# Performance work log

Measured on AMD Instinct MI355X. Metric: run time of the kernel, lower is better.

Reference implementation:

```python
import jax, jax.numpy as jnp
import numpy as np

GX, GY, NH = 480, 360, 32
EPS = 1e-5


def _bn(x, g, b):
    # torch BatchNorm1d training-mode stats over the point dimension
    m = jnp.mean(x, axis=0)
    v = jnp.mean((x - m) ** 2, axis=0)
    return g * (x - m) / jnp.sqrt(v + EPS) + b


def setup_inputs():
    key = jax.random.key(0)
    ks = jax.random.split(key, 24)
    B, N, F = 2, 120000, 7
    s = 0.02
    inp = {
        "pt_fea": jax.random.normal(ks[0], (B, N, F), jnp.float32),
        "xy_ind": jax.random.randint(ks[1], (B, N, 2), 0, 360, dtype=jnp.int32),
        "bn0_g": jnp.ones((7,), jnp.float32), "bn0_b": jnp.zeros((7,), jnp.float32),
        "W1": jax.random.normal(ks[2], (7, 64), jnp.float32) * s,  "b1": jnp.zeros((64,), jnp.float32),
        "bn1_g": jnp.ones((64,), jnp.float32), "bn1_b": jnp.zeros((64,), jnp.float32),
        "W2": jax.random.normal(ks[3], (64, 128), jnp.float32) * s, "b2": jnp.zeros((128,), jnp.float32),
        "bn2_g": jnp.ones((128,), jnp.float32), "bn2_b": jnp.zeros((128,), jnp.float32),
        "W3": jax.random.normal(ks[4], (128, 256), jnp.float32) * s, "b3": jnp.zeros((256,), jnp.float32),
        "bn3_g": jnp.ones((256,), jnp.float32), "bn3_b": jnp.zeros((256,), jnp.float32),
        "W4": jax.random.normal(ks[5], (256, 512), jnp.float32) * s, "b4": jnp.zeros((512,), jnp.float32),
        "W5": jax.random.normal(ks[6], (512, NH), jnp.float32) * s, "b5": jnp.zeros((NH,), jnp.float32),
    }
    return inp


def _forward_sample(fea, xy, bn0_g, bn0_b, W1, b1, bn1_g, bn1_b, W2, b2,
                    bn2_g, bn2_b, W3, b3, bn3_g, bn3_b, W4, b4, W5, b5):
    # Simplified PointNet: BN -> (Linear, BN, ReLU) x3 -> Linear
    x = _bn(fea, bn0_g, bn0_b)
    x = jax.nn.relu(_bn(x @ W1 + b1, bn1_g, bn1_b))
    x = jax.nn.relu(_bn(x @ W2 + b2, bn2_g, bn2_b))
    x = jax.nn.relu(_bn(x @ W3 + b3, bn3_g, bn3_b))
    x = x @ W4 + b4                              # [N, 512]
    # per-voxel segment max over flattened BEV cell id
    ids = xy[:, 0] * GY + xy[:, 1]               # [N]
    nseg = GX * GY
    seg = jax.ops.segment_max(x, ids, num_segments=nseg)   # [nseg, 512]
    cnt = jax.ops.segment_sum(jnp.ones(ids.shape[0], x.dtype), ids, num_segments=nseg)
    occ = (cnt > 0)[:, None]
    seg = jnp.where(occ, seg, 0.0)               # empty voxels -> 0 (scatter semantics)
    nh = jax.nn.relu(seg @ W5 + b5)              # fea_compression
    nh = jnp.where(occ, nh, 0.0)
    return nh.reshape(GX, GY, NH).transpose(2, 0, 1)  # [NH, GX, GY]


def reference(pt_fea, xy_ind, bn0_g, bn0_b, W1, b1, bn1_g, bn1_b, W2, b2,
              bn2_g, bn2_b, W3, b3, bn3_g, bn3_b, W4, b4, W5, b5):
    f = lambda fea, xy: _forward_sample(fea, xy, bn0_g, bn0_b, W1, b1, bn1_g, bn1_b,
                                        W2, b2, bn2_g, bn2_b, W3, b3, bn3_g, bn3_b,
                                        W4, b4, W5, b5)
    return jax.vmap(f)(pt_fea, xy_ind)           # [B, NH, GX, GY]
```

## Files before the change

### kernel.cpp

```cpp
#include <hip/hip_runtime.h>
#include <cstdint>

#define GXD 480
#define GYD 360
#define NHD 32
#define NPTS 120000
#define MPAD 120064
#define SEGR 129600
#define NSEG (GXD*GYD)
#define EPSB 1e-5f

using short8 = __attribute__((ext_vector_type(8))) short;
using f32x4  = __attribute__((ext_vector_type(4))) float;

__device__ __forceinline__ float bf2f(unsigned short u) {
    return __uint_as_float(((unsigned int)u) << 16);
}
__device__ __forceinline__ unsigned short f2bf(float f) {
    unsigned int u = __float_as_uint(f);
    u += 0x7fffu + ((u >> 16) & 1u);
    return (unsigned short)(u >> 16);
}
__device__ __forceinline__ unsigned int bnrelu_pack(unsigned int wv, float sc0, float sh0,
                                                    float sc1, float sh1)
{
    float lo = fmaxf(fmaf(bf2f((unsigned short)(wv & 0xffffu)), sc0, sh0), 0.f);
    float hi = fmaxf(fmaf(bf2f((unsigned short)(wv >> 16)), sc1, sh1), 0.f);
    return (unsigned int)f2bf(lo) | ((unsigned int)f2bf(hi) << 16);
}
__device__ __forceinline__ short8 bn_frag(short8 a, float4 s0, float4 s1,
                                          float4 h0, float4 h1)
{
    union { short8 v; uint4 u; } in, out;
    in.v = a;
    out.u.x = bnrelu_pack(in.u.x, s0.x, h0.x, s0.y, h0.y);
    out.u.y = bnrelu_pack(in.u.y, s0.z, h0.z, s0.w, h0.w);
    out.u.z = bnrelu_pack(in.u.z, s1.x, h1.x, s1.y, h1.y);
    out.u.w = bnrelu_pack(in.u.w, s1.z, h1.z, s1.w, h1.w);
    return out.v;
}

__device__ __forceinline__ void async16(const unsigned short* g, unsigned short* l)
{
    __builtin_amdgcn_global_load_lds(
        (const __attribute__((address_space(1))) unsigned int*)g,
        (__attribute__((address_space(3))) unsigned int*)l, 16, 0, 0);
}

__global__ __launch_bounds__(256) void bn0_stats_kernel(
    const float* __restrict__ fea, float* __restrict__ s0, float* __restrict__ q0)
{
    float s[7] = {0,0,0,0,0,0,0}, q[7] = {0,0,0,0,0,0,0};
    for (int p = blockIdx.x * 256 + threadIdx.x; p < NPTS; p += gridDim.x * 256) {
        const float* r = fea + (size_t)p * 7;
#pragma unroll
        for (int f = 0; f < 7; ++f) { float v = r[f]; s[f] += v; q[f] += v * v; }
    }
    __shared__ float red[256];
    int t = threadIdx.x;
#pragma unroll
    for (int f = 0; f < 7; ++f) {
        red[t] = s[f]; __syncthreads();
        for (int o = 128; o > 0; o >>= 1) {
            if (t < o) red[t] += red[t + o];
            __syncthreads();
        }
        if (t == 0) atomicAdd(&s0[f], red[0]);
        __syncthreads();
        red[t] = q[f]; __syncthreads();
        for (int o = 128; o > 0; o >>= 1) {
            if (t < o) red[t] += red[t + o];
            __syncthreads();
        }
        if (t == 0) atomicAdd(&q0[f], red[0]);
        __syncthreads();
    }
}

__global__ void prep0_kernel(const float* __restrict__ s0, const float* __restrict__ q0,
                             const float* __restrict__ g0, const float* __restrict__ b0,
                             const float* __restrict__ W1, const float* __restrict__ b1,
                             float* __restrict__ W1p, float* __restrict__ b1p)
{
    __shared__ float sc[7], sh[7];
    int t = threadIdx.x;
    if (t < 7) {
        float m = s0[t] / (float)NPTS;
        float v = q0[t] / (float)NPTS - m * m;
        float inv = 1.0f / sqrtf(fmaxf(v, 0.f) + EPSB);
        sc[t] = g0[t] * inv;
        sh[t] = b0[t] - m * g0[t] * inv;
    }
    __syncthreads();
    if (t < 64) {
        float acc = b1[t];
#pragma unroll
        for (int f = 0; f < 7; ++f) {
            W1p[f * 64 + t] = W1[f * 64 + t] * sc[f];
            acc += sh[f] * W1[f * 64 + t];
        }
        b1p[t] = acc;
    }
}

__global__ void prep_bn_kernel(const float* __restrict__ sum, const float* __restrict__ sq,
                               const float* __restrict__ g, const float* __restrict__ b,
                               float* __restrict__ sc, float* __restrict__ sh, int C)
{
    int c = blockIdx.x * blockDim.x + threadIdx.x;
    if (c < C) {
        float m = sum[c] / (float)NPTS;
        float v = sq[c] / (float)NPTS - m * m;
        float inv = 1.0f / sqrtf(fmaxf(v, 0.f) + EPSB);
        sc[c] = g[c] * inv;
        sh[c] = b[c] - m * g[c] * inv;
    }
}

__global__ __launch_bounds__(256) void wtrans_kernel(const float* __restrict__ W,
                                                     unsigned short* __restrict__ Wt,
                                                     int K, int N)
{
    int i = blockIdx.x * 256 + threadIdx.x;
    if (i < K * N) {
        int k = i / N, n = i % N;
        Wt[(size_t)n * K + k] = f2bf(W[i]);
    }
}

__global__ __launch_bounds__(256) void layer1_kernel(
    const float* __restrict__ fea, const float* __restrict__ W1p, const float* __restrict__ b1p,
    unsigned short* __restrict__ y1, float* __restrict__ sum1, float* __restrict__ sq1)
{
    __shared__ float Wl[448], bl[64];
    __shared__ float feaL[256 * 7];
    __shared__ float colsum[64], colsq[64];
    int t = threadIdx.x;
    int p0 = blockIdx.x * 256;
    for (int i = t; i < 448; i += 256) Wl[i] = W1p[i];
    if (t < 64) { bl[t] = b1p[t]; colsum[t] = 0.f; colsq[t] = 0.f; }
    int nval7 = (NPTS - p0) * 7;
    for (int i = t; i < 256 * 7; i += 256)
        feaL[i] = (i < nval7) ? fea[(size_t)p0 * 7 + i] : 0.f;
    __syncthreads();
    int cg = t & 7, pt = t >> 3;
    float s[8] = {}, q[8] = {};
#pragma unroll
    for (int it = 0; it < 8; ++it) {
        int row = it * 32 + pt;
        bool valid = (p0 + row) < NPTS;
        float f[7];
#pragma unroll
        for (int ff = 0; ff < 7; ++ff) f[ff] = feaL[row * 7 + ff];
        float vj[8];
#pragma unroll
        for (int j = 0; j < 8; ++j) {
            int c = cg * 8 + j;
            float v = bl[c];
#pragma unroll
            for (int ff = 0; ff < 7; ++ff) v = fmaf(f[ff], Wl[ff * 64 + c], v);
            vj[j] = v;
            if (valid) { s[j] += v; q[j] += v * v; }
        }
        uint4 ow;
        ow.x = (unsigned int)f2bf(vj[0]) | ((unsigned int)f2bf(vj[1]) << 16);
        ow.y = (unsigned int)f2bf(vj[2]) | ((unsigned int)f2bf(vj[3]) << 16);
        ow.z = (unsigned int)f2bf(vj[4]) | ((unsigned int)f2bf(vj[5]) << 16);
        ow.w = (unsigned int)f2bf(vj[6]) | ((unsigned int)f2bf(vj[7]) << 16);
        *(uint4*)(y1 + (size_t)(p0 + row) * 64 + cg * 8) = ow;
    }
#pragma unroll
    for (int off = 8; off < 64; off <<= 1) {
#pragma unroll
        for (int j = 0; j < 8; ++j) {
            s[j] += __shfl_xor(s[j], off);
            q[j] += __shfl_xor(q[j], off);
        }
    }
    if ((t & 63) < 8) {
#pragma unroll
        for (int j = 0; j < 8; ++j) {
            atomicAdd(&colsum[cg * 8 + j], s[j]);
            atomicAdd(&colsq[cg * 8 + j], q[j]);
        }
    }
    __syncthreads();
    if (t < 64) {
        atomicAdd(&sum1[t], colsum[t]);
        atomicAdd(&sq1[t], colsq[t]);
    }
}

template<int K, int NC, bool STATS>
__global__ __launch_bounds__(256) void gemm_quad(
    const unsigned short* __restrict__ A, const unsigned short* __restrict__ Wt,
    const float* __restrict__ scale, const float* __restrict__ shift,
    const float* __restrict__ bias, unsigned short* __restrict__ Y,
    float* __restrict__ osum, float* __restrict__ osq)
{
    __shared__ __align__(16) unsigned short lds[4 * 8192];
    __shared__ __align__(16) float scs[K], shs[K];
    __shared__ float colsum[128], colsq[128];
    int t = threadIdx.x;
    int w = t >> 6, ln = t & 63, quad = ln >> 4, lr = ln & 15;
    int wr = w >> 1, wc = w & 1;
    int mb = blockIdx.y * 128 + wr * 64;
    int cb = blockIdx.x * 128 + wc * 64;
    unsigned short* A0 = lds + w * 8192;
    unsigned short* B0 = A0 + 2048;
    unsigned short* A1 = A0 + 4096;
    unsigned short* B1 = A0 + 6144;

    for (int i = t; i < K; i += 256) { scs[i] = scale[i]; shs[i] = shift[i]; }
    if (STATS && t < 128) { colsum[t] = 0.f; colsq[t] = 0.f; }
    __syncthreads();

    const int grow = ln >> 2;
    const int swz = (((ln & 3) ^ ((ln >> 4) & 3)) << 3);
    const int rswz = ((quad ^ (lr >> 2)) << 3);

    f32x4 acc[4][4];
#pragma unroll
    for (int i = 0; i < 4; ++i)
#pragma unroll
        for (int j = 0; j < 4; ++j) acc[i][j] = (f32x4){0.f, 0.f, 0.f, 0.f};

#pragma unroll
    for (int i = 0; i < 4; ++i) {
        async16(A  + (size_t)(mb + i * 16 + grow) * K + swz, A0 + i * 512 + ln * 8);
        async16(Wt + (size_t)(cb + i * 16 + grow) * K + swz, B0 + i * 512 + ln * 8);
    }
#pragma unroll
    for (int i = 0; i < 4; ++i) {
        async16(A  + (size_t)(mb + i * 16 + grow) * K + 32 + swz, A1 + i * 512 + ln * 8);
        async16(Wt + (size_t)(cb + i * 16 + grow) * K + 32 + swz, B1 + i * 512 + ln * 8);
    }

#pragma unroll
    for (int r = 0; r < K / 32; ++r) {
        const int kt = r * 32;
        unsigned short* Acur = (r & 1) ? A1 : A0;
        unsigned short* Bcur = (r & 1) ? B1 : B0;
        int k0 = kt + quad * 8;
        float4 s0 = *(const float4*)&scs[k0];
        float4 s1 = *(const float4*)&scs[k0 + 4];
        float4 h0 = *(const float4*)&shs[k0];
        float4 h1 = *(const float4*)&shs[k0 + 4];
        if (r + 1 < K / 32)
            asm volatile("s_waitcnt vmcnt(8)" ::: "memory");
        else
            asm volatile("s_waitcnt vmcnt(0)" ::: "memory");
        short8 af[4], bfr[4];
#pragma unroll
        for (int mi = 0; mi < 4; ++mi)
            af[mi] = *(const short8*)&Acur[mi * 512 + lr * 32 + rswz];
#pragma unroll
        for (int ni = 0; ni < 4; ++ni)
            bfr[ni] = *(const short8*)&Bcur[ni * 512 + lr * 32 + rswz];
        asm volatile("s_waitcnt lgkmcnt(0)" ::: "memory");
        if (r + 2 < K / 32) {
            const int kn = kt + 64;
#pragma unroll
            for (int i = 0; i < 4; ++i) {
                async16(A  + (size_t)(mb + i * 16 + grow) * K + kn + swz,
                        Acur + i * 512 + ln * 8);
                async16(Wt + (size_t)(cb + i * 16 + grow) * K + kn + swz,
                        Bcur + i * 512 + ln * 8);
            }
        }
#pragma unroll
        for (int mi = 0; mi < 4; ++mi)
            af[mi] = bn_frag(af[mi], s0, s1, h0, h1);
#pragma unroll
        for (int mi = 0; mi < 4; ++mi)
#pragma unroll
            for (int ni = 0; ni < 4; ++ni)
                acc[mi][ni] = __builtin_amdgcn_mfma_f32_16x16x32_bf16(
                    af[mi], bfr[ni], acc[mi][ni], 0, 0, 0);
    }

    unsigned short* Cw = A0;
#pragma unroll
    for (int ni = 0; ni < 4; ++ni) {
        int col = ni * 16 + lr;
        float bv = bias[cb + col];
        float s = 0.f, q = 0.f;
#pragma unroll
        for (int mi = 0; mi < 4; ++mi) {
            int rb = mi * 16 + quad * 4;
#pragma unroll
            for (int r = 0; r < 4; ++r) {
                float v = acc[mi][ni][r] + bv;
                Cw[(rb + r) * 64 + col] = f2bf(v);
                if (STATS && (mb + rb + r) < NPTS) { s += v; q += v * v; }
            }
        }
        if (STATS) {
            atomicAdd(&colsum[wc * 64 + col], s);
            atomicAdd(&colsq[wc * 64 + col], q);
        }
    }
#pragma unroll
    for (int i = 0; i < 8; ++i) {
        int idx = i * 64 + ln;
        int row = idx >> 3, colq = (idx & 7) * 8;
        *(uint4*)(Y + (size_t)(mb + row) * NC + cb + colq) = *(const uint4*)&Cw[row * 64 + colq];
    }
    if (STATS) {
        __syncthreads();
        if (t < 128) {
            atomicAdd(&osum[blockIdx.x * 128 + t], colsum[t]);
            atomicAdd(&osq[blockIdx.x * 128 + t], colsq[t]);
        }
    }
}

__global__ __launch_bounds__(256) void hist_kernel(const int* __restrict__ xy,
                                                   int* __restrict__ cnt)
{
    int p = blockIdx.x * 256 + threadIdx.x;
    if (p < NPTS) {
        int id = xy[(size_t)p * 2] * GYD + xy[(size_t)p * 2 + 1];
        atomicAdd(&cnt[id], 1);
    }
}

__global__ __launch_bounds__(256) void scanA_kernel(const int* __restrict__ cnt,
                                                    int* __restrict__ csum)
{
    __shared__ int red[256];
    int t = threadIdx.x, base = blockIdx.x * 2048;
    int s = 0;
    for (int i = t; i < 2048; i += 256) {
        int idx = base + i;
        if (idx < SEGR) s += cnt[idx];
    }
    red[t] = s; __syncthreads();
    for (int o = 128; o > 0; o >>= 1) { if (t < o) red[t] += red[t + o]; __syncthreads(); }
    if (t == 0) csum[blockIdx.x] = red[0];
}

__global__ void scanB_kernel(int* __restrict__ csum, int* __restrict__ offs)
{
    if (threadIdx.x == 0) {
        int run = 0;
        for (int i = 0; i < 64; ++i) { int v = csum[i]; csum[i] = run; run += v; }
        offs[SEGR] = run;
    }
}

__global__ __launch_bounds__(256) void scanC_kernel(const int* __restrict__ cnt,
                                                    const int* __restrict__ csum,
                                                    int* __restrict__ offs,
                                                    int* __restrict__ cursor)
{
    __shared__ int red[256];
    int t = threadIdx.x, base = blockIdx.x * 2048;
    int v[8]; int s = 0;
#pragma unroll
    for (int i = 0; i < 8; ++i) {
        int idx = base + t * 8 + i;
        v[i] = (idx < SEGR) ? cnt[idx] : 0;
        s += v[i];
    }
    red[t] = s; __syncthreads();
    for (int o = 1; o < 256; o <<= 1) {
        int x = (t >= o) ? red[t - o] : 0;
        __syncthreads();
        red[t] += x;
        __syncthreads();
    }
    int run = red[t] - s + csum[blockIdx.x];
#pragma unroll
    for (int i = 0; i < 8; ++i) {
        int idx = base + t * 8 + i;
        if (idx < SEGR) { offs[idx] = run; cursor[idx] = run; }
        run += v[i];
    }
}

__global__ __launch_bounds__(256) void scatter_idx_kernel(const int* __restrict__ xy,
                                                          int* __restrict__ cursor,
                                                          int* __restrict__ order)
{
    int p = blockIdx.x * 256 + threadIdx.x;
    if (p < NPTS) {
        int id = xy[(size_t)p * 2] * GYD + xy[(size_t)p * 2 + 1];
        int pos = atomicAdd(&cursor[id], 1);
        order[pos] = p;
    }
}

__global__ __launch_bounds__(256) void segmax_l5_kernel(
    const unsigned short* __restrict__ y4g, const unsigned short* __restrict__ Wt5,
    const int* __restrict__ offs, const int* __restrict__ order,
    int g, float* __restrict__ E)
{
    __shared__ __align__(16) unsigned short seg[64 * 136];
    __shared__ __align__(16) unsigned short w5s[32 * 136];
    __shared__ int offs_s[65];
    int t = threadIdx.x;
    int c0 = blockIdx.x * 64;
    if (t < 65) offs_s[t] = offs[c0 + t];
    {
        int n = t >> 3, ko = (t & 7) * 16;
        *(uint4*)&w5s[n * 136 + ko]     = *(const uint4*)(Wt5 + (size_t)n * 512 + g * 128 + ko);
        *(uint4*)&w5s[n * 136 + ko + 8] = *(const uint4*)(Wt5 + (size_t)n * 512 + g * 128 + ko + 8);
    }
    __syncthreads();
    int cell = t >> 2, q = t & 3;
    float mx[32];
#pragma unroll
    for (int i = 0; i < 32; ++i) mx[i] = -3.0e38f;
    int jb = offs_s[cell], je = offs_s[cell + 1];
    for (int j = jb; j < je; ++j) {
        int p = order[j];
        const uint4* rp = (const uint4*)(y4g + (size_t)p * 128 + q * 32);
#pragma unroll
        for (int u = 0; u < 4; ++u) {
            uint4 vv = rp[u];
            unsigned int wv[4] = {vv.x, vv.y, vv.z, vv.w};
#pragma unroll
            for (int k2 = 0; k2 < 4; ++k2) {
                int idx = u * 8 + k2 * 2;
                mx[idx]     = fmaxf(mx[idx],     bf2f((unsigned short)(wv[k2] & 0xffffu)));
                mx[idx + 1] = fmaxf(mx[idx + 1], bf2f((unsigned short)(wv[k2] >> 16)));
            }
        }
    }
    bool empty = (jb == je);
#pragma unroll
    for (int i = 0; i < 16; ++i) {
        float lo = empty ? 0.f : mx[2 * i], hi = empty ? 0.f : mx[2 * i + 1];
        unsigned int pk = (unsigned int)f2bf(lo) | ((unsigned int)f2bf(hi) << 16);
        *(unsigned int*)&seg[cell * 136 + q * 32 + 2 * i] = pk;
    }
    __syncthreads();
    int lane = t & 63, w = t >> 6, quad = lane >> 4, lr = lane & 15;
    f32x4 acc[2];
    acc[0] = (f32x4){0.f, 0.f, 0.f, 0.f};
    acc[1] = (f32x4){0.f, 0.f, 0.f, 0.f};
#pragma unroll
    for (int kt = 0; kt < 4; ++kt) {
        short8 af = *(const short8*)&seg[(w * 16 + lr) * 136 + kt * 32 + quad * 8];
#pragma unroll
        for (int ni = 0; ni < 2; ++ni) {
            short8 bfr = *(const short8*)&w5s[(ni * 16 + lr) * 136 + kt * 32 + quad * 8];
            acc[ni] = __builtin_amdgcn_mfma_f32_16x16x32_bf16(af, bfr, acc[ni], 0, 0, 0);
        }
    }
#pragma unroll
    for (int ni = 0; ni < 2; ++ni) {
        int h = ni * 16 + lr;
#pragma unroll
        for (int r = 0; r < 4; ++r) {
            int cr = w * 16 + quad * 4 + r;
            float* ep = E + (size_t)(c0 + cr) * 32 + h;
            float v = acc[ni][r];
            if (g > 0) v += *ep;
            *ep = v;
        }
    }
}

__global__ __launch_bounds__(256) void out_kernel(
    const float* __restrict__ E, const int* __restrict__ cnt,
    const float* __restrict__ b5, float* __restrict__ out)
{
    int t = threadIdx.x;
    int c0 = blockIdx.x * 64;
    int lane = t & 63, hq = t >> 6;
    int cell = c0 + lane;
    if (c0 >= SEGR) {
#pragma unroll
        for (int j = 0; j < 8; ++j)
            out[(size_t)(hq * 8 + j) * NSEG + cell] = 0.f;
        return;
    }
    bool oc = cnt[cell] > 0;
    float4 e0 = *(const float4*)(E + (size_t)cell * 32 + hq * 8);
    float4 e1 = *(const float4*)(E + (size_t)cell * 32 + hq * 8 + 4);
    float r[8] = {e0.x, e0.y, e0.z, e0.w, e1.x, e1.y, e1.z, e1.w};
#pragma unroll
    for (int j = 0; j < 8; ++j) {
        float v = oc ? fmaxf(r[j] + b5[hq * 8 + j], 0.f) : 0.f;
        out[(size_t)(hq * 8 + j) * NSEG + cell] = v;
    }
}

extern "C" void kernel_launch(void* const* d_in, const int* in_sizes, int n_in,
                              void* d_out, int out_size, void* d_ws, size_t ws_size,
                              hipStream_t stream)
{
    const float* pt_fea = (const float*)d_in[0];
    const int*   xy_ind = (const int*)d_in[1];
    const float* bn0_g  = (const float*)d_in[2];
    const float* bn0_b  = (const float*)d_in[3];
    const float* W1     = (const float*)d_in[4];
    const float* b1     = (const float*)d_in[5];
    const float* bn1_g  = (const float*)d_in[6];
    const float* bn1_b  = (const float*)d_in[7];
    const float* W2     = (const float*)d_in[8];
    const float* b2     = (const float*)d_in[9];
    const float* bn2_g  = (const float*)d_in[10];
    const float* bn2_b  = (const float*)d_in[11];
    const float* W3     = (const float*)d_in[12];
    const float* b3     = (const float*)d_in[13];
    const float* bn3_g  = (const float*)d_in[14];
    const float* bn3_b  = (const float*)d_in[15];
    const float* W4     = (const float*)d_in[16];
    const float* b4     = (const float*)d_in[17];
    const float* W5     = (const float*)d_in[18];
    const float* b5     = (const float*)d_in[19];
    float* out = (float*)d_out;

    const size_t oY2   = 61472768;
    const size_t oE    = oY2 + (size_t)MPAD * 128 * 2;
    const size_t oCnt  = oE + (size_t)SEGR * 32 * 4;
    const size_t oOffs = oCnt + 518400;
    const size_t oCur  = oOffs + 518528;
    const size_t oOrd  = oCur + 518400;
    const size_t oCsum = oOrd + 480000;
    const size_t oSt   = oCsum + 512;
    const size_t oWt2  = oSt + 16384;
    const size_t oWt3  = oWt2 + 16384;
    const size_t oWt4  = oWt3 + 65536;
    const size_t oWt5  = oWt4 + 262144;

    unsigned short* y1   = (unsigned short*)d_ws;
    unsigned short* y3   = (unsigned short*)d_ws;
    unsigned short* y2   = (unsigned short*)((char*)d_ws + oY2);
    unsigned short* y4g  = (unsigned short*)((char*)d_ws + oY2);
    float*          E    = (float*)((char*)d_ws + oE);
    int*            cnt  = (int*)((char*)d_ws + oCnt);
    int*            offs = (int*)((char*)d_ws + oOffs);
    int*            cur  = (int*)((char*)d_ws + oCur);
    int*            ord  = (int*)((char*)d_ws + oOrd);
    int*            csum = (int*)((char*)d_ws + oCsum);
    float*          st   = (float*)((char*)d_ws + oSt);
    unsigned short* Wt2  = (unsigned short*)((char*)d_ws + oWt2);
    unsigned short* Wt3  = (unsigned short*)((char*)d_ws + oWt3);
    unsigned short* Wt4  = (unsigned short*)((char*)d_ws + oWt4);
    unsigned short* Wt5  = (unsigned short*)((char*)d_ws + oWt5);

    float* s0 = st + 0;     float* q0 = st + 8;
    float* W1p = st + 16;   float* b1p = st + 464;
    float* sum1 = st + 528; float* sq1 = st + 592; float* sc1 = st + 656; float* sh1 = st + 720;
    float* sum2 = st + 784; float* sq2 = st + 912; float* sc2 = st + 1040; float* sh2 = st + 1168;
    float* sum3 = st + 1296; float* sq3 = st + 1552; float* sc3 = st + 1808; float* sh3 = st + 2064;

    const int MB128 = MPAD / 128;

    wtrans_kernel<<<(64 * 128 + 255) / 256, 256, 0, stream>>>(W2, Wt2, 64, 128);
    wtrans_kernel<<<(128 * 256 + 255) / 256, 256, 0, stream>>>(W3, Wt3, 128, 256);
    wtrans_kernel<<<(256 * 512 + 255) / 256, 256, 0, stream>>>(W4, Wt4, 256, 512);
    wtrans_kernel<<<(512 * 32 + 255) / 256, 256, 0, stream>>>(W5, Wt5, 512, 32);

    for (int b = 0; b < 2; ++b) {
        const float* fea_b = pt_fea + (size_t)b * NPTS * 7;
        const int*   xy_b  = xy_ind + (size_t)b * NPTS * 2;
        float*       out_b = out + (size_t)b * NHD * NSEG;

        (void)hipMemsetAsync(st, 0, 2320 * sizeof(float), stream);
        (void)hipMemsetAsync(cnt, 0, (size_t)SEGR * 4, stream);

        bn0_stats_kernel<<<128, 256, 0, stream>>>(fea_b, s0, q0);
        prep0_kernel<<<1, 64, 0, stream>>>(s0, q0, bn0_g, bn0_b, W1, b1, W1p, b1p);
        layer1_kernel<<<MPAD / 256, 256, 0, stream>>>(fea_b, W1p, b1p, y1, sum1, sq1);
        prep_bn_kernel<<<1, 64, 0, stream>>>(sum1, sq1, bn1_g, bn1_b, sc1, sh1, 64);
        gemm_quad<64, 128, true><<<dim3(1, MB128), 256, 0, stream>>>(
            y1, Wt2, sc1, sh1, b2, y2, sum2, sq2);
        prep_bn_kernel<<<1, 128, 0, stream>>>(sum2, sq2, bn2_g, bn2_b, sc2, sh2, 128);
        gemm_quad<128, 256, true><<<dim3(2, MB128), 256, 0, stream>>>(
            y2, Wt3, sc2, sh2, b3, y3, sum3, sq3);
        prep_bn_kernel<<<1, 256, 0, stream>>>(sum3, sq3, bn3_g, bn3_b, sc3, sh3, 256);

        hist_kernel<<<(NPTS + 255) / 256, 256, 0, stream>>>(xy_b, cnt);
        scanA_kernel<<<64, 256, 0, stream>>>(cnt, csum);
        scanB_kernel<<<1, 64, 0, stream>>>(csum, offs);
        scanC_kernel<<<64, 256, 0, stream>>>(cnt, csum, offs, cur);
        scatter_idx_kernel<<<(NPTS + 255) / 256, 256, 0, stream>>>(xy_b, cur, ord);

        for (int g = 0; g < 4; ++g) {
            gemm_quad<256, 128, false><<<dim3(1, MB128), 256, 0, stream>>>(
                y3, Wt4 + (size_t)g * 128 * 256, sc3, sh3, b4 + g * 128, y4g,
                nullptr, nullptr);
            segmax_l5_kernel<<<SEGR / 64, 256, 0, stream>>>(y4g, Wt5, offs, ord, g, E);
        }
        out_kernel<<<NSEG / 64, 256, 0, stream>>>(E, cnt, b5, out_b);
    }
}
```

Measured before the change: 838.1 us.

## Move BN+ReLU out of GEMM prologue into standalone elementwise passes

Removes the per-fragment BN-scale/shift and ReLU from the GEMM inner loop and instead applies BN+ReLU in place on y1, y2 and y3 with a new vectorized elementwise kernel. This also drops the LDS XOR swizzle in the GEMM and uses a packed bf16 convert instruction. The aim is to shorten the MFMA loop, especially since y3 was re-normalized four times across the W4 column groups. In exchange it adds extra full read/write passes over the activations and may bring back LDS bank conflicts now that the swizzle is gone.

```diff
diff --git a/kernel.cpp b/kernel.cpp
--- a/kernel.cpp
+++ b/kernel.cpp
@@ -24,20 +24,13 @@
 __device__ __forceinline__ unsigned int bnrelu_pack(unsigned int wv, float sc0, float sh0,
                                                     float sc1, float sh1)
 {
-    float lo = fmaxf(fmaf(bf2f((unsigned short)(wv & 0xffffu)), sc0, sh0), 0.f);
-    float hi = fmaxf(fmaf(bf2f((unsigned short)(wv >> 16)), sc1, sh1), 0.f);
-    return (unsigned int)f2bf(lo) | ((unsigned int)f2bf(hi) << 16);
-}
-__device__ __forceinline__ short8 bn_frag(short8 a, float4 s0, float4 s1,
-                                          float4 h0, float4 h1)
-{
-    union { short8 v; uint4 u; } in, out;
-    in.v = a;
-    out.u.x = bnrelu_pack(in.u.x, s0.x, h0.x, s0.y, h0.y);
-    out.u.y = bnrelu_pack(in.u.y, s0.z, h0.z, s0.w, h0.w);
-    out.u.z = bnrelu_pack(in.u.z, s1.x, h1.x, s1.y, h1.y);
-    out.u.w = bnrelu_pack(in.u.w, s1.z, h1.z, s1.w, h1.w);
-    return out.v;
+    float lo = __uint_as_float(wv << 16);
+    float hi = __uint_as_float(wv & 0xffff0000u);
+    lo = fmaxf(fmaf(lo, sc0, sh0), 0.f);
+    hi = fmaxf(fmaf(hi, sc1, sh1), 0.f);
+    unsigned int r;
+    asm("v_cvt_pk_bf16_f32 %0, %1, %2" : "=v"(r) : "v"(lo), "v"(hi));
+    return r;
 }
 
 __device__ __forceinline__ void async16(const unsigned short* g, unsigned short* l)
@@ -114,6 +107,32 @@
         float inv = 1.0f / sqrtf(fmaxf(v, 0.f) + EPSB);
         sc[c] = g[c] * inv;
         sh[c] = b[c] - m * g[c] * inv;
+    }
+}
+
+template<int C>
+__global__ __launch_bounds__(256) void bnrelu_kernel(
+    unsigned short* __restrict__ Y,
+    const float* __restrict__ sc, const float* __restrict__ sh)
+{
+    __shared__ float scs[C], shs[C];
+    int t = threadIdx.x;
+    for (int i = t; i < C; i += 256) { scs[i] = sc[i]; shs[i] = sh[i]; }
+    __syncthreads();
+    const size_t total8 = (size_t)MPAD * C / 8;
+    for (size_t i = (size_t)blockIdx.x * 256 + t; i < total8; i += (size_t)gridDim.x * 256) {
+        int c0 = (int)((i * 8) & (size_t)(C - 1));
+        uint4 v = *(const uint4*)(Y + i * 8);
+        float4 s0 = *(const float4*)&scs[c0];
+        float4 s1 = *(const float4*)&scs[c0 + 4];
+        float4 h0 = *(const float4*)&shs[c0];
+        float4 h1 = *(const float4*)&shs[c0 + 4];
+        uint4 o;
+        o.x = bnrelu_pack(v.x, s0.x, h0.x, s0.y, h0.y);
+        o.y = bnrelu_pack(v.y, s0.z, h0.z, s0.w, h0.w);
+        o.z = bnrelu_pack(v.z, s1.x, h1.x, s1.y, h1.y);
+        o.w = bnrelu_pack(v.w, s1.z, h1.z, s1.w, h1.w);
+        *(uint4*)(Y + i * 8) = o;
     }
 }
 
@@ -194,12 +213,10 @@
 template<int K, int NC, bool STATS>
 __global__ __launch_bounds__(256) void gemm_quad(
     const unsigned short* __restrict__ A, const unsigned short* __restrict__ Wt,
-    const float* __restrict__ scale, const float* __restrict__ shift,
     const float* __restrict__ bias, unsigned short* __restrict__ Y,
     float* __restrict__ osum, float* __restrict__ osq)
 {
     __shared__ __align__(16) unsigned short lds[4 * 8192];
-    __shared__ __align__(16) float scs[K], shs[K];
     __shared__ float colsum[128], colsq[128];
     int t = threadIdx.x;
     int w = t >> 6, ln = t & 63, quad = ln >> 4, lr = ln & 15;
@@ -211,13 +228,11 @@
     unsigned short* A1 = A0 + 4096;
     unsigned short* B1 = A0 + 6144;
 
-    for (int i = t; i < K; i += 256) { scs[i] = scale[i]; shs[i] = shift[i]; }
     if (STATS && t < 128) { colsum[t] = 0.f; colsq[t] = 0.f; }
     __syncthreads();
 
     const int grow = ln >> 2;
-    const int swz = (((ln & 3) ^ ((ln >> 4) & 3)) << 3);
-    const int rswz = ((quad ^ (lr >> 2)) << 3);
+    const int koff = (ln & 3) * 8;
 
     f32x4 acc[4][4];
 #pragma unroll
@@ -227,13 +242,13 @@
 
 #pragma unroll
     for (int i = 0; i < 4; ++i) {
-        async16(A  + (size_t)(mb + i * 16 + grow) * K + swz, A0 + i * 512 + ln * 8);
-        async16(Wt + (size_t)(cb + i * 16 + grow) * K + swz, B0 + i * 512 + ln * 8);
+        async16(A  + (size_t)(mb + i * 16 + grow) * K + koff, A0 + i * 512 + ln * 8);
+        async16(Wt + (size_t)(cb + i * 16 + grow) * K + koff, B0 + i * 512 + ln * 8);
     }
 #pragma unroll
     for (int i = 0; i < 4; ++i) {
-        async16(A  + (size_t)(mb + i * 16 + grow) * K + 32 + swz, A1 + i * 512 + ln * 8);
-        async16(Wt + (size_t)(cb + i * 16 + grow) * K + 32 + swz, B1 + i * 512 + ln * 8);
+        async16(A  + (size_t)(mb + i * 16 + grow) * K + 32 + koff, A1 + i * 512 + ln * 8);
+        async16(Wt + (size_t)(cb + i * 16 + grow) * K + 32 + koff, B1 + i * 512 + ln * 8);
     }
 
 #pragma unroll
@@ -241,11 +256,6 @@
         const int kt = r * 32;
         unsigned short* Acur = (r & 1) ? A1 : A0;
         unsigned short* Bcur = (r & 1) ? B1 : B0;
-        int k0 = kt + quad * 8;
-        float4 s0 = *(const float4*)&scs[k0];
-        float4 s1 = *(const float4*)&scs[k0 + 4];
-        float4 h0 = *(const float4*)&shs[k0];
-        float4 h1 = *(const float4*)&shs[k0 + 4];
         if (r + 1 < K / 32)
             asm volatile("s_waitcnt vmcnt(8)" ::: "memory");
         else
@@ -253,24 +263,21 @@
         short8 af[4], bfr[4];
 #pragma unroll
         for (int mi = 0; mi < 4; ++mi)
-            af[mi] = *(const short8*)&Acur[mi * 512 + lr * 32 + rswz];
+            af[mi] = *(const short8*)&Acur[mi * 512 + lr * 32 + quad * 8];
 #pragma unroll
         for (int ni = 0; ni < 4; ++ni)
-            bfr[ni] = *(const short8*)&Bcur[ni * 512 + lr * 32 + rswz];
+            bfr[ni] = *(const short8*)&Bcur[ni * 512 + lr * 32 + quad * 8];
         asm volatile("s_waitcnt lgkmcnt(0)" ::: "memory");
         if (r + 2 < K / 32) {
             const int kn = kt + 64;
 #pragma unroll
             for (int i = 0; i < 4; ++i) {
-                async16(A  + (size_t)(mb + i * 16 + grow) * K + kn + swz,
+                async16(A  + (size_t)(mb + i * 16 + grow) * K + kn + koff,
                         Acur + i * 512 + ln * 8);
-                async16(Wt + (size_t)(cb + i * 16 + grow) * K + kn + swz,
+                async16(Wt + (size_t)(cb + i * 16 + grow) * K + kn + koff,
                         Bcur + i * 512 + ln * 8);
             }
         }
-#pragma unroll
-        for (int mi = 0; mi < 4; ++mi)
-            af[mi] = bn_frag(af[mi], s0, s1, h0, h1);
 #pragma unroll
         for (int mi = 0; mi < 4; ++mi)
 #pragma unroll
@@ -568,12 +575,15 @@
         prep0_kernel<<<1, 64, 0, stream>>>(s0, q0, bn0_g, bn0_b, W1, b1, W1p, b1p);
         layer1_kernel<<<MPAD / 256, 256, 0, stream>>>(fea_b, W1p, b1p, y1, sum1, sq1);
         prep_bn_kernel<<<1, 64, 0, stream>>>(sum1, sq1, bn1_g, bn1_b, sc1, sh1, 64);
+        bnrelu_kernel<64><<<1024, 256, 0, stream>>>(y1, sc1, sh1);
         gemm_quad<64, 128, true><<<dim3(1, MB128), 256, 0, stream>>>(
-            y1, Wt2, sc1, sh1, b2, y2, sum2, sq2);
+            y1, Wt2, b2, y2, sum2, sq2);
         prep_bn_kernel<<<1, 128, 0, stream>>>(sum2, sq2, bn2_g, bn2_b, sc2, sh2, 128);
+        bnrelu_kernel<128><<<2048, 256, 0, stream>>>(y2, sc2, sh2);
         gemm_quad<128, 256, true><<<dim3(2, MB128), 256, 0, stream>>>(
-            y2, Wt3, sc2, sh2, b3, y3, sum3, sq3);
+            y2, Wt3, b3, y3, sum3, sq3);
         prep_bn_kernel<<<1, 256, 0, stream>>>(sum3, sq3, bn3_g, bn3_b, sc3, sh3, 256);
+        bnrelu_kernel<256><<<2048, 256, 0, stream>>>(y3, sc3, sh3);
 
         hist_kernel<<<(NPTS + 255) / 256, 256, 0, stream>>>(xy_b, cnt);
         scanA_kernel<<<64, 256, 0, stream>>>(cnt, csum);
@@ -583,7 +593,7 @@
 
         for (int g = 0; g < 4; ++g) {
             gemm_quad<256, 128, false><<<dim3(1, MB128), 256, 0, stream>>>(
-                y3, Wt4 + (size_t)g * 128 * 256, sc3, sh3, b4 + g * 128, y4g,
+                y3, Wt4 + (size_t)g * 128 * 256, b4 + g * 128, y4g,
                 nullptr, nullptr);
             segmax_l5_kernel<<<SEGR / 64, 256, 0, stream>>>(y4g, Wt5, offs, ord, g, E);
         }
```

Result: no change. 847.4 us (+1.1%).
